# Performance work log

Measured on AMD Instinct MI355X. Metric: run time of the kernel, lower is better.

Reference implementation:

```python
import jax, jax.numpy as jnp
import numpy as np

V, H, B = 64, 128, 16384  # num_visible, num_hidden = alpha*V, batch of spin configs
ISCALE = 0.001


def setup_inputs() -> dict:
    key = jax.random.key(0)
    k1, k2, k3, k4 = jax.random.split(key, 4)
    x = jax.random.normal(k1, (B, V), dtype=jnp.float32)
    weight_1 = jax.random.normal(k2, (V, H), dtype=jnp.float32) * ISCALE
    weight_2 = jax.random.normal(k3, (H, V, V), dtype=jnp.float32) * (ISCALE / 10.0)
    hidden_bias = jax.random.normal(k4, (H,), dtype=jnp.float32) * ISCALE
    return {"x": x, "weight_1": weight_1, "weight_2": weight_2, "hidden_bias": hidden_bias}


def reference(x, weight_1, weight_2, hidden_bias):
    b, v = x.shape
    h = weight_2.shape[0]
    # order-1 term: (B,V) @ (V,H) -> (B,H)
    w1 = x @ weight_1
    # order-2 term: outer product of spins per sample, contracted with weight_2.
    # vis_ij: (B,V,V) flattened to (B,V*V); weight_2 flattened to (H,V*V) -> GEMM.
    vis_ij = jnp.einsum('mi,mj->mij', x, x).reshape(b, v * v)
    w2 = (vis_ij @ weight_2.reshape(h, v * v).T) * 0.5
    act = jnp.cos(hidden_bias + w1 + w2)  # (B,H)
    psi = jnp.prod(act, axis=-1)          # (B,)
    return psi
```

## Files before the change

kernel.cpp:

```cpp
#include <hip/hip_runtime.h>
#include <hip/hip_bf16.h>
#include <cstdint>

#define NV 64
#define NH 128
#define NB 16384
#define NCHUNK 37
#define FRAG_ELEMS (NCHUNK * 8192)

typedef __bf16 bf16x8_t __attribute__((ext_vector_type(8)));
typedef float f32x4_t __attribute__((ext_vector_type(4)));
typedef float f32x2_t __attribute__((ext_vector_type(2)));
typedef uint32_t u32x4_t __attribute__((ext_vector_type(4)));
typedef uint32_t u32x2_t __attribute__((ext_vector_type(2)));

__device__ __forceinline__ uint32_t bf16_rne(float f) {
  uint32_t u = __float_as_uint(f);
  return (u + 0x7fffu + ((u >> 16) & 1u)) >> 16;
}

__global__ void cvt_kernel(const float* __restrict__ w1f,
                           const float* __restrict__ w2f,
                           uint16_t* __restrict__ frag) {
  int tg = blockIdx.x * 256 + threadIdx.x;
  int l = tg & 63, fh = (tg >> 6) & 7, c2 = tg >> 9;
  int chunk = c2 >> 1, jh = c2 & 1;
  int h = fh * 16 + (l & 15);
  int kb = jh * 32 + (l >> 4) * 8;
  uint32_t o16[8];
#pragma unroll
  for (int t = 0; t < 8; ++t) {
    int slot = kb + t;
    float v;
    if (chunk < 8) {
      int i = chunk * 8 + (slot >> 3), j = chunk * 8 + (slot & 7);
      v = 0.5f * w2f[h * 4096 + i * 64 + j];
    } else if (chunk < 36) {
      int o = chunk - 8, I = 0;
      while (o >= 7 - I) { o -= 7 - I; ++I; }
      int J = I + 1 + o;
      int i = I * 8 + (slot >> 3), j = J * 8 + (slot & 7);
      v = 0.5f * (w2f[h * 4096 + i * 64 + j] + w2f[h * 4096 + j * 64 + i]);
    } else {
      v = w1f[slot * 128 + h];
    }
    o16[t] = bf16_rne(v);
  }
  uint4 o;
  o.x = (o16[1] << 16) | o16[0];
  o.y = (o16[3] << 16) | o16[2];
  o.z = (o16[5] << 16) | o16[4];
  o.w = (o16[7] << 16) | o16[6];
  *(uint4*)(frag + ((size_t)(c2 * 8 + fh) << 9) + l * 8) = o;
}

__launch_bounds__(512, 4)
__global__ void rbm_kernel(const float* __restrict__ xg,
                           const float* __restrict__ biasg,
                           const __hip_bfloat16* __restrict__ frag,
                           float* __restrict__ outg) {
  __shared__ __align__(16) float xtile[32 * 76];
  __shared__ float part[4][32];

  const int tid  = threadIdx.x;
  const int wv   = tid >> 6;
  const int wm   = wv & 1;
  const int hq   = wv >> 1;
  const int lane = tid & 63;
  const int c15  = lane & 15;
  const int q    = lane >> 4;
  const int mblk = blockIdx.x * 32;

  constexpr int CI[36] = {0,1,2,3,4,5,6,7, 0,0,0,0,0,0,0, 1,1,1,1,1,1,
                          2,2,2,2,2, 3,3,3,3, 4,4,4, 5,5, 6};
  constexpr int CJ[36] = {0,1,2,3,4,5,6,7, 1,2,3,4,5,6,7, 2,3,4,5,6,7,
                          3,4,5,6,7, 4,5,6,7, 5,6,7, 6,7, 7};

  {
    int row = tid >> 4, col4 = (tid & 15) * 4;
    const float* p = xg + (size_t)(mblk + row) * NV + col4;
    *(float4*)(&xtile[row * 76 + col4]) = *(const float4*)p;
  }
  __syncthreads();

  const float* sx = &xtile[(wm * 16 + c15) * 76];
  f32x2_t xb[32];
#pragma unroll
  for (int g = 0; g < 8; ++g) {
    float4 a = *(const float4*)(sx + g * 8);
    float4 b4 = *(const float4*)(sx + g * 8 + 4);
    xb[g * 4 + 0] = f32x2_t{a.x, a.y};
    xb[g * 4 + 1] = f32x2_t{a.z, a.w};
    xb[g * 4 + 2] = f32x2_t{b4.x, b4.y};
    xb[g * 4 + 3] = f32x2_t{b4.z, b4.w};
  }

  const __hip_bfloat16* pw = frag + (size_t)hq * 1024 + lane * 8;

  f32x4_t acc[2];
#pragma unroll
  for (int ih = 0; ih < 2; ++ih)
    acc[ih] = (f32x4_t)0.0f;

  bf16x8_t b[4];
#pragma unroll
  for (int jh = 0; jh < 2; ++jh)
#pragma unroll
    for (int ih = 0; ih < 2; ++ih)
      b[jh * 2 + ih] = *(const bf16x8_t*)(pw + jh * 4096 + ih * 512);

#pragma unroll
  for (int c = 0; c < 36; ++c) {
    const int I = CI[c], J = CJ[c];
    bf16x8_t afrag[2];
#pragma unroll
    for (int jh = 0; jh < 2; ++jh) {
      float s = sx[I * 8 + jh * 4 + q];
      const f32x2_t s2 = f32x2_t{s, s};
      u32x4_t adv;
#pragma unroll
      for (int tt = 0; tt < 4; ++tt) {
        f32x2_t pr = s2 * xb[J * 4 + tt];
        u32x2_t u = __builtin_bit_cast(u32x2_t, pr);
        adv[tt] = __builtin_amdgcn_perm(u[1], u[0], 0x07060302);
      }
      afrag[jh] = __builtin_bit_cast(bf16x8_t, adv);
    }
    const __hip_bfloat16* pn = pw + (size_t)(c + 1) * 8192;
#pragma unroll
    for (int jh = 0; jh < 2; ++jh)
#pragma unroll
      for (int ih = 0; ih < 2; ++ih) {
        acc[ih] = __builtin_amdgcn_mfma_f32_16x16x32_bf16(
            afrag[jh], b[jh * 2 + ih], acc[ih], 0, 0, 0);
        b[jh * 2 + ih] = *(const bf16x8_t*)(pn + jh * 4096 + ih * 512);
      }
  }

#pragma unroll
  for (int jh = 0; jh < 2; ++jh) {
    float4 a = *(const float4*)(sx + jh * 32 + q * 8);
    float4 b4 = *(const float4*)(sx + jh * 32 + q * 8 + 4);
    const float pr[4][2] = {{a.x, a.y}, {a.z, a.w}, {b4.x, b4.y}, {b4.z, b4.w}};
    u32x4_t adv;
#pragma unroll
    for (int tt = 0; tt < 4; ++tt)
      adv[tt] = __builtin_amdgcn_perm(__float_as_uint(pr[tt][1]),
                                      __float_as_uint(pr[tt][0]), 0x07060302);
    bf16x8_t af = __builtin_bit_cast(bf16x8_t, adv);
#pragma unroll
    for (int ih = 0; ih < 2; ++ih)
      acc[ih] = __builtin_amdgcn_mfma_f32_16x16x32_bf16(
          af, b[jh * 2 + ih], acc[ih], 0, 0, 0);
  }

  float bs[2];
#pragma unroll
  for (int ih = 0; ih < 2; ++ih)
    bs[ih] = biasg[hq * 32 + ih * 16 + c15];

  const float INV2PI = 0.15915494309189535f;
  float prod[4];
#pragma unroll
  for (int r = 0; r < 4; ++r) {
    float c0 = __builtin_amdgcn_cosf((acc[0][r] + bs[0]) * INV2PI);
    float c1 = __builtin_amdgcn_cosf((acc[1][r] + bs[1]) * INV2PI);
    prod[r] = c0 * c1;
  }

#pragma unroll
  for (int ofs = 1; ofs < 16; ofs <<= 1)
#pragma unroll
    for (int r = 0; r < 4; ++r)
      prod[r] *= __shfl_xor(prod[r], ofs, 16);

  if (c15 == 0) {
#pragma unroll
    for (int r = 0; r < 4; ++r)
      part[hq][wm * 16 + q * 4 + r] = prod[r];
  }
  __syncthreads();
  if (tid < 32) {
    float f = part[0][tid] * part[1][tid] * part[2][tid] * part[3][tid];
    outg[mblk + tid] = f;
  }
}

extern "C" void kernel_launch(void* const* d_in, const int* in_sizes, int n_in,
                              void* d_out, int out_size, void* d_ws, size_t ws_size,
                              hipStream_t stream) {
  const float* x   = (const float*)d_in[0];
  const float* w1f = (const float*)d_in[1];
  const float* w2f = (const float*)d_in[2];
  const float* hb  = (const float*)d_in[3];
  float* out = (float*)d_out;
  uint16_t* frag = (uint16_t*)d_ws;
  (void)in_sizes; (void)n_in; (void)out_size; (void)ws_size;

  cvt_kernel<<<148, 256, 0, stream>>>(w1f, w2f, frag);
  rbm_kernel<<<NB / 32, 512, 0, stream>>>(
      x, hb, (const __hip_bfloat16*)frag, out);
}
```

Baseline: 87.13 us.

## Retile RBM kernel to 64 rows per block with 64 hidden units per wave

Each block now handles 64 samples instead of 32, with 4 row-waves by 2 hidden-waves, and each wave computes 4 hidden tiles instead of 2. Each A fragment built from x outer products is reused across twice as many MFMAs, so the per-sample VALU work of building fragments drops. Weight fragment loads per wave double, so register pressure rises; launch bounds are lowered to 2 blocks per SM to allow that. There are half as many blocks (256), which may under-fill the GPU.

```diff
diff --git a/kernel.cpp b/kernel.cpp
--- a/kernel.cpp
+++ b/kernel.cpp
@@ -54,22 +54,22 @@
   *(uint4*)(frag + ((size_t)(c2 * 8 + fh) << 9) + l * 8) = o;
 }
 
-__launch_bounds__(512, 4)
+__launch_bounds__(512, 2)
 __global__ void rbm_kernel(const float* __restrict__ xg,
                            const float* __restrict__ biasg,
                            const __hip_bfloat16* __restrict__ frag,
                            float* __restrict__ outg) {
-  __shared__ __align__(16) float xtile[32 * 76];
-  __shared__ float part[4][32];
+  __shared__ __align__(16) float xtile[64 * 76];
+  __shared__ float part[2][64];
 
   const int tid  = threadIdx.x;
   const int wv   = tid >> 6;
-  const int wm   = wv & 1;
-  const int hq   = wv >> 1;
+  const int wm   = wv & 3;
+  const int hq   = wv >> 2;
   const int lane = tid & 63;
   const int c15  = lane & 15;
   const int q    = lane >> 4;
-  const int mblk = blockIdx.x * 32;
+  const int mblk = blockIdx.x * 64;
 
   constexpr int CI[36] = {0,1,2,3,4,5,6,7, 0,0,0,0,0,0,0, 1,1,1,1,1,1,
                           2,2,2,2,2, 3,3,3,3, 4,4,4, 5,5, 6};
@@ -77,9 +77,12 @@
                           3,4,5,6,7, 4,5,6,7, 5,6,7, 6,7, 7};
 
   {
-    int row = tid >> 4, col4 = (tid & 15) * 4;
-    const float* p = xg + (size_t)(mblk + row) * NV + col4;
-    *(float4*)(&xtile[row * 76 + col4]) = *(const float4*)p;
+    int row = tid >> 3, grp = tid & 7;
+    const float* p = xg + (size_t)(mblk + row) * NV + grp * 8;
+    float4 a = *(const float4*)(p);
+    float4 b4 = *(const float4*)(p + 4);
+    *(float4*)(&xtile[row * 76 + grp * 8]) = a;
+    *(float4*)(&xtile[row * 76 + grp * 8 + 4]) = b4;
   }
   __syncthreads();
 
@@ -95,24 +98,24 @@
     xb[g * 4 + 3] = f32x2_t{b4.z, b4.w};
   }
 
-  const __hip_bfloat16* pw = frag + (size_t)hq * 1024 + lane * 8;
-
-  f32x4_t acc[2];
-#pragma unroll
-  for (int ih = 0; ih < 2; ++ih)
+  const __hip_bfloat16* pw = frag + (size_t)hq * 2048 + lane * 8;
+
+  f32x4_t acc[4];
+#pragma unroll
+  for (int ih = 0; ih < 4; ++ih)
     acc[ih] = (f32x4_t)0.0f;
 
-  bf16x8_t b[4];
+  bf16x8_t b[2][4];
 #pragma unroll
   for (int jh = 0; jh < 2; ++jh)
 #pragma unroll
-    for (int ih = 0; ih < 2; ++ih)
-      b[jh * 2 + ih] = *(const bf16x8_t*)(pw + jh * 4096 + ih * 512);
+    for (int ih = 0; ih < 4; ++ih)
+      b[jh][ih] = *(const bf16x8_t*)(pw + jh * 4096 + ih * 512);
 
 #pragma unroll
   for (int c = 0; c < 36; ++c) {
     const int I = CI[c], J = CJ[c];
-    bf16x8_t afrag[2];
+    const __hip_bfloat16* pn = pw + (size_t)(c + 1) * 8192;
 #pragma unroll
     for (int jh = 0; jh < 2; ++jh) {
       float s = sx[I * 8 + jh * 4 + q];
@@ -124,17 +127,14 @@
         u32x2_t u = __builtin_bit_cast(u32x2_t, pr);
         adv[tt] = __builtin_amdgcn_perm(u[1], u[0], 0x07060302);
       }
-      afrag[jh] = __builtin_bit_cast(bf16x8_t, adv);
+      bf16x8_t afrag = __builtin_bit_cast(bf16x8_t, adv);
+#pragma unroll
+      for (int ih = 0; ih < 4; ++ih) {
+        acc[ih] = __builtin_amdgcn_mfma_f32_16x16x32_bf16(
+            afrag, b[jh][ih], acc[ih], 0, 0, 0);
+        b[jh][ih] = *(const bf16x8_t*)(pn + jh * 4096 + ih * 512);
+      }
     }
-    const __hip_bfloat16* pn = pw + (size_t)(c + 1) * 8192;
-#pragma unroll
-    for (int jh = 0; jh < 2; ++jh)
-#pragma unroll
-      for (int ih = 0; ih < 2; ++ih) {
-        acc[ih] = __builtin_amdgcn_mfma_f32_16x16x32_bf16(
-            afrag[jh], b[jh * 2 + ih], acc[ih], 0, 0, 0);
-        b[jh * 2 + ih] = *(const bf16x8_t*)(pn + jh * 4096 + ih * 512);
-      }
   }
 
 #pragma unroll
@@ -149,15 +149,15 @@
                                       __float_as_uint(pr[tt][0]), 0x07060302);
     bf16x8_t af = __builtin_bit_cast(bf16x8_t, adv);
 #pragma unroll
-    for (int ih = 0; ih < 2; ++ih)
+    for (int ih = 0; ih < 4; ++ih)
       acc[ih] = __builtin_amdgcn_mfma_f32_16x16x32_bf16(
-          af, b[jh * 2 + ih], acc[ih], 0, 0, 0);
-  }
-
-  float bs[2];
-#pragma unroll
-  for (int ih = 0; ih < 2; ++ih)
-    bs[ih] = biasg[hq * 32 + ih * 16 + c15];
+          af, b[jh][ih], acc[ih], 0, 0, 0);
+  }
+
+  float bs[4];
+#pragma unroll
+  for (int ih = 0; ih < 4; ++ih)
+    bs[ih] = biasg[hq * 64 + ih * 16 + c15];
 
   const float INV2PI = 0.15915494309189535f;
   float prod[4];
@@ -165,7 +165,9 @@
   for (int r = 0; r < 4; ++r) {
     float c0 = __builtin_amdgcn_cosf((acc[0][r] + bs[0]) * INV2PI);
     float c1 = __builtin_amdgcn_cosf((acc[1][r] + bs[1]) * INV2PI);
-    prod[r] = c0 * c1;
+    float c2 = __builtin_amdgcn_cosf((acc[2][r] + bs[2]) * INV2PI);
+    float c3 = __builtin_amdgcn_cosf((acc[3][r] + bs[3]) * INV2PI);
+    prod[r] = (c0 * c1) * (c2 * c3);
   }
 
 #pragma unroll
@@ -180,8 +182,8 @@
       part[hq][wm * 16 + q * 4 + r] = prod[r];
   }
   __syncthreads();
-  if (tid < 32) {
-    float f = part[0][tid] * part[1][tid] * part[2][tid] * part[3][tid];
+  if (tid < 64) {
+    float f = part[0][tid] * part[1][tid];
     outg[mblk + tid] = f;
   }
 }
@@ -198,6 +200,6 @@
   (void)in_sizes; (void)n_in; (void)out_size; (void)ws_size;
 
   cvt_kernel<<<148, 256, 0, stream>>>(w1f, w2f, frag);
-  rbm_kernel<<<NB / 32, 512, 0, stream>>>(
+  rbm_kernel<<<NB / 64, 512, 0, stream>>>(
       x, hb, (const __hip_bfloat16*)frag, out);
 }
```

Measured after the change: 89.73 us. +3.0%, slower.
